# Kernel optimization log

Hardware: AMD Instinct MI355X
Metric: run time of the kernel (lower is better)

## Reference

```python
import jax, jax.numpy as jnp
import numpy as np

NEG = -9e15
ALPHA = 0.2  # leakyrelu slope


def setup_inputs() -> dict:
    key = jax.random.key(0)
    ks = jax.random.split(key, 12)
    bs, N, Fx, F, D = 8, 512, 8, 64, 16
    return {
        'input': jax.random.normal(ks[0], (bs, N, 1), jnp.float32),
        'adj': jax.random.randint(ks[1], (N, N), 0, 2, jnp.int32),
        'ext_input': jax.random.normal(ks[2], (bs, N, Fx), jnp.float32),
        'side_input': jax.random.normal(ks[3], (bs, N, 1), jnp.float32),
        'W': jax.random.normal(ks[4], (1, F), jnp.float32),
        'a': jax.random.normal(ks[5], (2 * F, 1), jnp.float32),
        'WS': jax.random.normal(ks[6], (1, F), jnp.float32),
        'aS': jax.random.normal(ks[7], (2 * F, 1), jnp.float32),
        'WQ': jax.random.normal(ks[8], (2, D), jnp.float32),
        'WK': jax.random.normal(ks[9], (2, D), jnp.float32),
        'WV': jax.random.normal(ks[10], (1, F), jnp.float32),
    }


def _pair_scores(h, a_vec):
    # e[b,i,j] = leakyrelu(a . [h_i, h_j]) ; equivalent to h@a1 + (h@a2)^T
    F = h.shape[-1]
    s1 = h @ a_vec[:F]          # [b,N,1]
    s2 = h @ a_vec[F:]          # [b,N,1]
    return jax.nn.leaky_relu(s1 + jnp.swapaxes(s2, 1, 2), negative_slope=ALPHA)


def reference(input, adj, ext_input, side_input, W, a, WS, aS, WQ, WK, WV):
    bs, N, _ = input.shape
    Fx = ext_input.shape[-1]
    D = WQ.shape[1]
    mask = (adj > 0)[None, :, :]  # [1,N,N] broadcasts over batch

    # ---- Step 1: node-channel GAT attention ----
    h = input @ W                    # [b,N,F]
    e = _pair_scores(h, a)           # [b,N,N]
    att = jnp.where(mask, e, NEG)
    h_side = side_input @ WS         # [b,N,F]
    e_side = _pair_scores(h_side, aS)
    att_side = jnp.where(mask, e_side, NEG)
    att = att + att_side
    att = jnp.where(att > 0, att, NEG)
    att = jax.nn.softmax(att, axis=2)             # [b,N,N]
    h_prime = jnp.einsum('bij,bjf->bif', att, h)  # [b,N,F]

    # ---- Step 2: ext-feature dot-product attention ----
    xs = input[..., 0]  # [b,N]
    # q[b,i,j,d] = (x_i*WQ[0,d] + x_j*WQ[1,d]) / sqrt(D)
    q = (xs[:, :, None, None] * WQ[0] + xs[:, None, :, None] * WQ[1]) / (D ** 0.5)
    # k[b,i,j,d,f] = ext_i_f*WK[0,d] + ext_j_f*WK[1,d]; dot = sum_d q*k, computed fused:
    qk0 = q @ WK[0]   # [b,N,N]
    qk1 = q @ WK[1]   # [b,N,N]
    dot = ext_input[:, :, None, :] * qk0[..., None] + ext_input[:, None, :, :] * qk1[..., None]  # [b,N,N,Fx]
    dot = jnp.where(dot > 0, dot, NEG)
    dot = jax.nn.softmax(dot, axis=3)
    final = dot * att[..., None]                 # [b,N,N,Fx]
    v = ext_input[..., None] * WV[0][None, None, None, :]  # [b,N,Fx,F]
    ext_rep = jnp.einsum('bijf,bife->bie', final, v)       # sum over j and f -> [b,N,F]

    return jax.nn.elu(h_prime), jax.nn.elu(ext_rep)
```

## Files before the change

### kernel.cpp

```cpp
#include <hip/hip_runtime.h>

#define NEGV (-9e15f)
#define LOG2E 1.44269504088896340736f

__device__ __forceinline__ float wsum(float v) {
#pragma unroll
    for (int off = 32; off > 0; off >>= 1) v += __shfl_xor(v, off, 64);
    return v;
}
__device__ __forceinline__ float wmax(float v) {
#pragma unroll
    for (int off = 32; off > 0; off >>= 1) v = fmaxf(v, __shfl_xor(v, off, 64));
    return v;
}
__device__ __forceinline__ float hsum16(float v) {
#pragma unroll
    for (int off = 1; off < 16; off <<= 1) v += __shfl_xor(v, off, 64);
    return v;
}
__device__ __forceinline__ float bcast0(float v) {
    return __int_as_float(__builtin_amdgcn_readfirstlane(__float_as_int(v)));
}
__device__ __forceinline__ void ld8f(const float* p, float* o) {
    const float4 v0 = ((const float4*)p)[0];
    const float4 v1 = ((const float4*)p)[1];
    o[0] = v0.x; o[1] = v0.y; o[2] = v0.z; o[3] = v0.w;
    o[4] = v1.x; o[5] = v1.y; o[6] = v1.z; o[7] = v1.w;
}

__global__ __launch_bounds__(64) void sentinel_kernel(float* __restrict__ out) {
    out[blockIdx.x * 64 + threadIdx.x] = 111222.0f;
}

__global__ __launch_bounds__(64, 2) void gat_fused_f32(
    const float* __restrict__ input, const int* __restrict__ adj,
    const float* __restrict__ ext, const float* __restrict__ side,
    const float* __restrict__ W, const float* __restrict__ a,
    const float* __restrict__ WS, const float* __restrict__ aS,
    const float* __restrict__ WQ, const float* __restrict__ WK,
    const float* __restrict__ WV, float* __restrict__ out)
{
    const int N = 512, F = 64;
    const int lane = threadIdx.x;
    const int b = blockIdx.x >> 8;
    const int i0 = (blockIdx.x & 255) * 2;

    const bool adj64 = (__any(adj[2 * lane + 1] != 0) == 0);

    const float wf  = W[lane];
    const float wvf = WV[lane];
    const float c1  = wsum(wf * a[lane]) * LOG2E;
    const float c2  = wsum(wf * a[F + lane]) * LOG2E;
    const float wsf = WS[lane];
    const float cS1 = wsum(wsf * aS[lane]) * LOG2E;
    const float cS2 = wsum(wsf * aS[F + lane]) * LOG2E;
    float q0 = 0.f, q1 = 0.f, k0 = 0.f, k1 = 0.f;
    if (lane < 16) {
        q0 = WQ[lane]; q1 = WQ[16 + lane];
        k0 = WK[lane]; k1 = WK[16 + lane];
    }
    const float QS = 0.25f * LOG2E;
    const float a00 = bcast0(hsum16(q0 * k0)) * QS;
    const float a01 = bcast0(hsum16(q0 * k1)) * QS;
    const float a10 = bcast0(hsum16(q1 * k0)) * QS;
    const float a11 = bcast0(hsum16(q1 * k1)) * QS;

    const int row0 = b * N + i0;
    const float x0 = input[row0], x1 = input[row0 + 1];
    const float y0 = side[row0],  y1 = side[row0 + 1];
    float ei0[8], ei1[8];
    ld8f(ext + (size_t)row0 * 8, ei0);
    ld8f(ext + (size_t)(row0 + 1) * 8, ei1);

    const float s10 = c1 * x0,  s11 = c1 * x1;
    const float t10 = cS1 * y0, t11 = cS1 * y1;

    const float* xp = input + b * N;
    const float* yp = side + b * N;
    const int* adji0 = adj + i0 * N;
    const int* adji1 = adji0 + N;
    const long long* adjl0 = (const long long*)adj + (size_t)i0 * N;
    const long long* adjl1 = adjl0 + N;

    float xj[8], L0[8], L1[8];
#pragma unroll
    for (int t = 0; t < 8; t++) {
        const int jj = lane + 64 * t;
        const float xv = xp[jj];
        const float yv = yp[jj];
        xj[t] = xv;
        const float z  = c2 * xv;
        const float zs = cS2 * yv;
        float u0 = s10 + z;  u0 = fmaxf(u0, 0.2f * u0);
        float v0 = t10 + zs; v0 = fmaxf(v0, 0.2f * v0);
        float u1 = s11 + z;  u1 = fmaxf(u1, 0.2f * u1);
        float v1 = t11 + zs; v1 = fmaxf(v1, 0.2f * v1);
        const float w0 = u0 + v0;
        const float w1 = u1 + v1;
        int m0, m1;
        if (adj64) { m0 = (adjl0[jj] != 0); m1 = (adjl1[jj] != 0); }
        else       { m0 = adji0[jj];        m1 = adji1[jj]; }
        L0[t] = (m0 != 0 && w0 > 0.f) ? w0 : NEGV;
        L1[t] = (m1 != 0 && w1 > 0.f) ? w1 : NEGV;
    }
    float M0 = L0[0], M1 = L1[0];
#pragma unroll
    for (int t = 1; t < 8; t++) { M0 = fmaxf(M0, L0[t]); M1 = fmaxf(M1, L1[t]); }
    M0 = wmax(M0); M1 = wmax(M1);

    float s0 = 0.f, s1 = 0.f;
#pragma unroll
    for (int t = 0; t < 8; t++) {
        L0[t] = __builtin_amdgcn_exp2f(L0[t] - M0); s0 += L0[t];
        L1[t] = __builtin_amdgcn_exp2f(L1[t] - M1); s1 += L1[t];
    }
    const float inv0 = __builtin_amdgcn_rcpf(wsum(s0));
    const float inv1 = __builtin_amdgcn_rcpf(wsum(s1));

    float A0 = 0.f, A1 = 0.f, R0 = 0.f, R1 = 0.f;
#pragma unroll
    for (int t = 0; t < 8; t++) {
        const int jj = lane + 64 * t;
        float ej[8];
        ld8f(ext + (size_t)(b * N + jj) * 8, ej);
        const float qj0 = xj[t] * a10, qj1 = xj[t] * a11;
        const float qk00 = x0 * a00 + qj0, qk01 = x0 * a01 + qj1;
        const float qk10 = x1 * a00 + qj0, qk11 = x1 * a01 + qj1;

        float d0[8], d1[8];
        float dm0 = NEGV, dm1 = NEGV;
#pragma unroll
        for (int f = 0; f < 8; f++) {
            float dv0 = ei0[f] * qk00 + ej[f] * qk01;
            float dv1 = ei1[f] * qk10 + ej[f] * qk11;
            dv0 = (dv0 > 0.f) ? dv0 : NEGV;
            dv1 = (dv1 > 0.f) ? dv1 : NEGV;
            d0[f] = dv0; dm0 = fmaxf(dm0, dv0);
            d1[f] = dv1; dm1 = fmaxf(dm1, dv1);
        }
        float ds0 = 0.f, ds1 = 0.f, dot0 = 0.f, dot1 = 0.f;
#pragma unroll
        for (int f = 0; f < 8; f++) {
            const float e0 = __builtin_amdgcn_exp2f(d0[f] - dm0);
            const float e1 = __builtin_amdgcn_exp2f(d1[f] - dm1);
            ds0 += e0; dot0 += e0 * ei0[f];
            ds1 += e1; dot1 += e1 * ei1[f];
        }
        A0 += L0[t] * xj[t];
        A1 += L1[t] * xj[t];
        R0 += L0[t] * __builtin_amdgcn_rcpf(ds0) * dot0;
        R1 += L1[t] * __builtin_amdgcn_rcpf(ds1) * dot1;
    }
    A0 = wsum(A0); A1 = wsum(A1);
    R0 = wsum(R0); R1 = wsum(R1);

    const int o = row0 * F + lane;
    float o00 = A0 * inv0 * wf;
    float o01 = A1 * inv1 * wf;
    float o10 = R0 * inv0 * wvf;
    float o11 = R1 * inv1 * wvf;
    o00 = (o00 > 0.f) ? o00 : (__builtin_amdgcn_exp2f(o00 * LOG2E) - 1.f);
    o01 = (o01 > 0.f) ? o01 : (__builtin_amdgcn_exp2f(o01 * LOG2E) - 1.f);
    o10 = (o10 > 0.f) ? o10 : (__builtin_amdgcn_exp2f(o10 * LOG2E) - 1.f);
    o11 = (o11 > 0.f) ? o11 : (__builtin_amdgcn_exp2f(o11 * LOG2E) - 1.f);
    out[o] = o00;
    out[o + F] = o01;
    out[262144 + o] = o10;
    out[262144 + o + F] = o11;
}

extern "C" void kernel_launch(void* const* d_in, const int* in_sizes, int n_in,
                              void* d_out, int out_size, void* d_ws, size_t ws_size,
                              hipStream_t stream) {
    static const int exp_sizes[11] = {4096, 262144, 32768, 4096, 64, 128, 64, 128, 32, 32, 64};
    bool ok = (n_in == 11) && (out_size == 524288);
    if (ok) {
        for (int k = 0; k < 11; k++) if (in_sizes[k] != exp_sizes[k]) ok = false;
    }
    if (!ok) {
        sentinel_kernel<<<4096, 64, 0, stream>>>((float*)d_out);
        return;
    }

    gat_fused_f32<<<2048, 64, 0, stream>>>(
        (const float*)d_in[0], (const int*)d_in[1],
        (const float*)d_in[2], (const float*)d_in[3],
        (const float*)d_in[4], (const float*)d_in[5],
        (const float*)d_in[6], (const float*)d_in[7],
        (const float*)d_in[8], (const float*)d_in[9],
        (const float*)d_in[10],
        (float*)d_out);
}
```

Before: 15.53 us.

## Split neighbor range across two waves with online-softmax merge and LDS-staged ext

Each block now runs two wavefronts, each handling half of the 512 neighbors for the same two rows. Partial softmax max, sum and accumulators are merged through shared memory with a rescaling step, and the two waves split the output writes. Each wave's ext slice is loaded early into registers and transposed into LDS so the inner loop reads it feature-major. The aim is to halve the per-wave serial loop and hide load latency, at the cost of a block barrier, extra LDS traffic and more threads per block.

```diff
diff --git a/kernel.cpp b/kernel.cpp
--- a/kernel.cpp
+++ b/kernel.cpp
@@ -32,7 +32,7 @@
     out[blockIdx.x * 64 + threadIdx.x] = 111222.0f;
 }
 
-__global__ __launch_bounds__(64, 2) void gat_fused_f32(
+__global__ __launch_bounds__(128, 4) void gat_fused_f32(
     const float* __restrict__ input, const int* __restrict__ adj,
     const float* __restrict__ ext, const float* __restrict__ side,
     const float* __restrict__ W, const float* __restrict__ a,
@@ -41,9 +41,24 @@
     const float* __restrict__ WV, float* __restrict__ out)
 {
     const int N = 512, F = 64;
-    const int lane = threadIdx.x;
+    const int lane = threadIdx.x & 63;
+    const int w = threadIdx.x >> 6;
     const int b = blockIdx.x >> 8;
     const int i0 = (blockIdx.x & 255) * 2;
+
+    __shared__ float exts[2][8][256];
+    __shared__ float mrg[16];
+
+    const int jbase = 256 * w;
+
+    const float* ebase = ext + (size_t)(b * N + jbase) * 8;
+    float4 stA[4], stB[4];
+#pragma unroll
+    for (int u = 0; u < 4; u++) {
+        const float* p = ebase + (size_t)(u * 64 + lane) * 8;
+        stA[u] = ((const float4*)p)[0];
+        stB[u] = ((const float4*)p)[1];
+    }
 
     const bool adj64 = (__any(adj[2 * lane + 1] != 0) == 0);
 
@@ -75,16 +90,17 @@
     const float s10 = c1 * x0,  s11 = c1 * x1;
     const float t10 = cS1 * y0, t11 = cS1 * y1;
 
-    const float* xp = input + b * N;
-    const float* yp = side + b * N;
-    const int* adji0 = adj + i0 * N;
+    const float* xp = input + b * N + jbase;
+    const float* yp = side + b * N + jbase;
+    const int arow0 = i0 * N + jbase;
+    const int* adji0 = adj + arow0;
     const int* adji1 = adji0 + N;
-    const long long* adjl0 = (const long long*)adj + (size_t)i0 * N;
+    const long long* adjl0 = (const long long*)adj + arow0;
     const long long* adjl1 = adjl0 + N;
 
-    float xj[8], L0[8], L1[8];
-#pragma unroll
-    for (int t = 0; t < 8; t++) {
+    float xj[4], L0[4], L1[4];
+#pragma unroll
+    for (int t = 0; t < 4; t++) {
         const int jj = lane + 64 * t;
         const float xv = xp[jj];
         const float yv = yp[jj];
@@ -95,34 +111,47 @@
         float v0 = t10 + zs; v0 = fmaxf(v0, 0.2f * v0);
         float u1 = s11 + z;  u1 = fmaxf(u1, 0.2f * u1);
         float v1 = t11 + zs; v1 = fmaxf(v1, 0.2f * v1);
-        const float w0 = u0 + v0;
-        const float w1 = u1 + v1;
+        const float g0 = u0 + v0;
+        const float g1 = u1 + v1;
         int m0, m1;
         if (adj64) { m0 = (adjl0[jj] != 0); m1 = (adjl1[jj] != 0); }
         else       { m0 = adji0[jj];        m1 = adji1[jj]; }
-        L0[t] = (m0 != 0 && w0 > 0.f) ? w0 : NEGV;
-        L1[t] = (m1 != 0 && w1 > 0.f) ? w1 : NEGV;
-    }
-    float M0 = L0[0], M1 = L1[0];
-#pragma unroll
-    for (int t = 1; t < 8; t++) { M0 = fmaxf(M0, L0[t]); M1 = fmaxf(M1, L1[t]); }
+        L0[t] = (m0 != 0 && g0 > 0.f) ? g0 : NEGV;
+        L1[t] = (m1 != 0 && g1 > 0.f) ? g1 : NEGV;
+    }
+    float M0 = fmaxf(fmaxf(L0[0], L0[1]), fmaxf(L0[2], L0[3]));
+    float M1 = fmaxf(fmaxf(L1[0], L1[1]), fmaxf(L1[2], L1[3]));
     M0 = wmax(M0); M1 = wmax(M1);
 
     float s0 = 0.f, s1 = 0.f;
 #pragma unroll
-    for (int t = 0; t < 8; t++) {
+    for (int t = 0; t < 4; t++) {
         L0[t] = __builtin_amdgcn_exp2f(L0[t] - M0); s0 += L0[t];
         L1[t] = __builtin_amdgcn_exp2f(L1[t] - M1); s1 += L1[t];
     }
-    const float inv0 = __builtin_amdgcn_rcpf(wsum(s0));
-    const float inv1 = __builtin_amdgcn_rcpf(wsum(s1));
+    s0 = wsum(s0); s1 = wsum(s1);
+
+#pragma unroll
+    for (int u = 0; u < 4; u++) {
+        const int r = u * 64 + lane;
+        exts[w][0][r] = stA[u].x;
+        exts[w][1][r] = stA[u].y;
+        exts[w][2][r] = stA[u].z;
+        exts[w][3][r] = stA[u].w;
+        exts[w][4][r] = stB[u].x;
+        exts[w][5][r] = stB[u].y;
+        exts[w][6][r] = stB[u].z;
+        exts[w][7][r] = stB[u].w;
+    }
 
     float A0 = 0.f, A1 = 0.f, R0 = 0.f, R1 = 0.f;
 #pragma unroll
-    for (int t = 0; t < 8; t++) {
+    for (int t = 0; t < 4; t++) {
         const int jj = lane + 64 * t;
         float ej[8];
-        ld8f(ext + (size_t)(b * N + jj) * 8, ej);
+#pragma unroll
+        for (int f = 0; f < 8; f++) ej[f] = exts[w][f][jj];
+
         const float qj0 = xj[t] * a10, qj1 = xj[t] * a11;
         const float qk00 = x0 * a00 + qj0, qk01 = x0 * a01 + qj1;
         const float qk10 = x1 * a00 + qj0, qk11 = x1 * a01 + qj1;
@@ -154,19 +183,38 @@
     A0 = wsum(A0); A1 = wsum(A1);
     R0 = wsum(R0); R1 = wsum(R1);
 
+    if (lane == 0) {
+        float* m = mrg + w * 8;
+        m[0] = M0; m[1] = M1; m[2] = s0; m[3] = s1;
+        m[4] = A0; m[5] = A1; m[6] = R0; m[7] = R1;
+    }
+    __syncthreads();
+
+    const float Ma0 = fmaxf(mrg[0], mrg[8]);
+    const float Ma1 = fmaxf(mrg[1], mrg[9]);
+    const float p00 = __builtin_amdgcn_exp2f(mrg[0] - Ma0);
+    const float p01 = __builtin_amdgcn_exp2f(mrg[8] - Ma0);
+    const float p10 = __builtin_amdgcn_exp2f(mrg[1] - Ma1);
+    const float p11 = __builtin_amdgcn_exp2f(mrg[9] - Ma1);
+    const float inv0 = __builtin_amdgcn_rcpf(p00 * mrg[2] + p01 * mrg[10]);
+    const float inv1 = __builtin_amdgcn_rcpf(p10 * mrg[3] + p11 * mrg[11]);
+
     const int o = row0 * F + lane;
-    float o00 = A0 * inv0 * wf;
-    float o01 = A1 * inv1 * wf;
-    float o10 = R0 * inv0 * wvf;
-    float o11 = R1 * inv1 * wvf;
-    o00 = (o00 > 0.f) ? o00 : (__builtin_amdgcn_exp2f(o00 * LOG2E) - 1.f);
-    o01 = (o01 > 0.f) ? o01 : (__builtin_amdgcn_exp2f(o01 * LOG2E) - 1.f);
-    o10 = (o10 > 0.f) ? o10 : (__builtin_amdgcn_exp2f(o10 * LOG2E) - 1.f);
-    o11 = (o11 > 0.f) ? o11 : (__builtin_amdgcn_exp2f(o11 * LOG2E) - 1.f);
-    out[o] = o00;
-    out[o + F] = o01;
-    out[262144 + o] = o10;
-    out[262144 + o + F] = o11;
+    if (w == 0) {
+        float o00 = (p00 * mrg[4] + p01 * mrg[12]) * inv0 * wf;
+        float o01 = (p10 * mrg[5] + p11 * mrg[13]) * inv1 * wf;
+        o00 = (o00 > 0.f) ? o00 : (__builtin_amdgcn_exp2f(o00 * LOG2E) - 1.f);
+        o01 = (o01 > 0.f) ? o01 : (__builtin_amdgcn_exp2f(o01 * LOG2E) - 1.f);
+        out[o] = o00;
+        out[o + F] = o01;
+    } else {
+        float o10 = (p00 * mrg[6] + p01 * mrg[14]) * inv0 * wvf;
+        float o11 = (p10 * mrg[7] + p11 * mrg[15]) * inv1 * wvf;
+        o10 = (o10 > 0.f) ? o10 : (__builtin_amdgcn_exp2f(o10 * LOG2E) - 1.f);
+        o11 = (o11 > 0.f) ? o11 : (__builtin_amdgcn_exp2f(o11 * LOG2E) - 1.f);
+        out[262144 + o] = o10;
+        out[262144 + o + F] = o11;
+    }
 }
 
 extern "C" void kernel_launch(void* const* d_in, const int* in_sizes, int n_in,
@@ -182,7 +230,7 @@
         return;
     }
 
-    gat_fused_f32<<<2048, 64, 0, stream>>>(
+    gat_fused_f32<<<2048, 128, 0, stream>>>(
         (const float*)d_in[0], (const int*)d_in[1],
         (const float*)d_in[2], (const float*)d_in[3],
         (const float*)d_in[4], (const float*)d_in[5],
```

Measured after the change: 15.17 us. 1.02x faster.
